# Kernel tuning notes

Measured on AMD Instinct MI355X. Metric: run time of the kernel, lower is better.

## Reference

```python
import jax, jax.numpy as jnp
import numpy as np

BSZ = 5
PROJ = 1000
DET = 513
IMG = 362
NPIX = IMG * IMG          # 131044
NNZ = 20_000_000


def setup_inputs() -> dict:
    key = jax.random.key(0)
    k1, k2, k3, k4 = jax.random.split(key, 4)
    filtered_sino = jax.random.normal(k1, (BSZ, PROJ, DET, 1), dtype=jnp.float32)
    sp_vals = jax.random.uniform(k2, (NNZ,), dtype=jnp.float32)
    sp_rows = jax.random.randint(k3, (NNZ,), 0, NPIX, dtype=jnp.int32)
    sp_cols = jax.random.randint(k4, (NNZ,), 0, PROJ * DET, dtype=jnp.int32)
    return {"filtered_sino": filtered_sino, "sp_vals": sp_vals,
            "sp_rows": sp_rows, "sp_cols": sp_cols}


def reference(filtered_sino, sp_vals, sp_rows, sp_cols):
    # Flatten each sinogram to [PROJ*DET] (row-major: proj then det, as tf.reshape).
    sino_flat = filtered_sino.reshape(BSZ, PROJ * DET)

    def back_project(s):  # s: [PROJ*DET] -> [NPIX]
        # sparse COO @ dense vector: out[row] += val * s[col]
        return jax.ops.segment_sum(sp_vals * s[sp_cols], sp_rows, num_segments=NPIX)

    rec = jax.vmap(back_project)(sino_flat)          # [BSZ, NPIX]
    # sens_image = back-projection of an all-ones sinogram
    sens = jax.ops.segment_sum(sp_vals, sp_rows, num_segments=NPIX)  # [NPIX]
    out = (rec / sens).reshape(BSZ, IMG, IMG, 1)
    return out
```

## Files before the change

### kernel.cpp

```cpp
#include <hip/hip_runtime.h>
#include <hip/hip_fp16.h>

#define BSZ  5
#define PROJ 1000
#define DET  513
#define IMG  362
#define NPIX (IMG * IMG)
#define SINO (PROJ * DET)
#define NNZ  20000000

#define NSHARD     4
#define SHARD_COLS (SINO / NSHARD)
#define RB_SHIFT   10
#define RB_PX      1024
#define NRBIN      128
#define NBIN       (NRBIN * NSHARD)

#define SCAT_BLOCKS  256
#define CHUNK        78128
#define TILE         4096
#define SC2_THREADS  512

#define CAP        200
#define OVF_CAP    65536

#define ACC_THREADS  512

#define FXSCALE 16384.0f
#define FXINV   (1.0f / 16384.0f)
#define FXB     262144
#define NTAG    0x1000000u

typedef int      i32x4 __attribute__((ext_vector_type(4)));
typedef float    f32x4 __attribute__((ext_vector_type(4)));
typedef unsigned u32x4 __attribute__((ext_vector_type(4)));

__device__ __forceinline__ unsigned lds_off(const void* p) {
    return (unsigned)(size_t)p;
}
__device__ __forceinline__ void ds_add_u64_nr(unsigned off, unsigned long long v) {
    asm volatile("ds_add_u64 %0, %1" :: "v"(off), "v"(v) : "memory");
}
__device__ __forceinline__ void lgkm_drain() {
    asm volatile("s_waitcnt lgkmcnt(0)" ::: "memory");
}

__device__ __forceinline__ int bin_of(int row, int col) {
    return ((row >> RB_SHIFT) << 2) | (col / SHARD_COLS);
}


__global__ void k_sino_bf16(const float* __restrict__ sino, u32x4* __restrict__ sino_b) {
    const int c = blockIdx.x * blockDim.x + threadIdx.x;
    if (c < SINO) {
        unsigned b[5];
#pragma unroll
        for (int k = 0; k < 5; ++k) {
            const unsigned u = __float_as_uint(sino[(size_t)k * SINO + c]);
            b[k] = (u + 0x7FFFu + ((u >> 16) & 1u)) >> 16;
        }
        u32x4 o;
        o.x = b[0] | (b[1] << 16);
        o.y = b[2] | (b[3] << 16);
        o.z = b[4];
        o.w = 0u;
        sino_b[c] = o;
    }
}

__global__ __launch_bounds__(SC2_THREADS) void k_scatter(
        const float* __restrict__ vals, const int* __restrict__ rows,
        const int* __restrict__ cols,
        unsigned* __restrict__ recA, unsigned short* __restrict__ recB,
        unsigned* __restrict__ gcnt,
        unsigned long long* __restrict__ ovf, unsigned* __restrict__ ovf_n) {
    __shared__ unsigned cnt[NBIN];
    __shared__ unsigned toff[NBIN];
    __shared__ unsigned ebase[NBIN];
    __shared__ unsigned bs2[NBIN];
    __shared__ unsigned wsum[8];
    __shared__ unsigned long long sdata[TILE];
    const int t = threadIdx.x;
    const int lane = t & 63;
    const int lo = blockIdx.x * CHUNK;
    const int hi = (lo + CHUNK < NNZ) ? lo + CHUNK : NNZ;
    if (lo >= hi) return;

    if (t < NBIN) {
        bs2[t] = ((unsigned)blockIdx.x * NBIN + (unsigned)t) * CAP;
        cnt[t] = 0u;
    }

    i32x4 sr0, sr1, sq0, sq1; f32x4 sv0, sv1;
    {
        const int n0 = (lo + TILE < hi) ? TILE : (hi - lo);
        if (t * 8 < n0) {
            const int i4 = (lo + t * 8) >> 2;
            sr0 = __builtin_nontemporal_load(((const i32x4*)rows) + i4);
            sr1 = __builtin_nontemporal_load(((const i32x4*)rows) + i4 + 1);
            sq0 = __builtin_nontemporal_load(((const i32x4*)cols) + i4);
            sq1 = __builtin_nontemporal_load(((const i32x4*)cols) + i4 + 1);
            sv0 = __builtin_nontemporal_load(((const f32x4*)vals) + i4);
            sv1 = __builtin_nontemporal_load(((const f32x4*)vals) + i4 + 1);
        }
    }
    __syncthreads();

    for (int tb = lo; tb < hi; tb += TILE) {
        const int n = (tb + TILE < hi) ? TILE : (hi - tb);
        const bool act = (t * 8) < n;

        const i32x4 cr0 = sr0, cr1 = sr1, cq0 = sq0, cq1 = sq1;
        const f32x4 cv0 = sv0, cv1 = sv1;

        const int ntb = tb + TILE;
        if (ntb < hi) {
            const int nn = (ntb + TILE < hi) ? TILE : (hi - ntb);
            if (t * 8 < nn) {
                const int i4 = (ntb + t * 8) >> 2;
                sr0 = __builtin_nontemporal_load(((const i32x4*)rows) + i4);
                sr1 = __builtin_nontemporal_load(((const i32x4*)rows) + i4 + 1);
                sq0 = __builtin_nontemporal_load(((const i32x4*)cols) + i4);
                sq1 = __builtin_nontemporal_load(((const i32x4*)cols) + i4 + 1);
                sv0 = __builtin_nontemporal_load(((const f32x4*)vals) + i4);
                sv1 = __builtin_nontemporal_load(((const f32x4*)vals) + i4 + 1);
            }
        }

        unsigned long long r8[8];
        unsigned sl[8];
        if (act) {
#pragma unroll
            for (int k = 0; k < 8; ++k) {
                const int rr = (k < 4) ? cr0[k] : cr1[k - 4];
                const int qq = (k < 4) ? cq0[k] : cq1[k - 4];
                const float vf = (k < 4) ? cv0[k] : cv1[k - 4];
                const unsigned bn = (unsigned)bin_of(rr, qq);
                const unsigned vh = (unsigned)__half_as_ushort(__float2half(vf));
                r8[k] = ((unsigned long long)bn << 55)
                      | ((unsigned long long)(unsigned)(rr & (RB_PX - 1)) << 45)
                      | ((unsigned long long)(unsigned)qq << 26)
                      | (unsigned long long)vh;
                sl[k] = atomicAdd(&cnt[bn], 1u);
            }
        }
        __syncthreads();

        unsigned x = 0u, incl = 0u;
        if (t < NBIN) {
            x = cnt[t];
            incl = x;
#pragma unroll
            for (int o = 1; o < 64; o <<= 1) {
                const unsigned y = __shfl_up(incl, (unsigned)o, 64);
                if (lane >= o) incl += y;
            }
            if (lane == 63) wsum[t >> 6] = incl;
        }
        __syncthreads();
        if (t < NBIN) {
            unsigned wo = 0u;
            const int w = t >> 6;
            for (int k = 0; k < w; ++k) wo += wsum[k];
            const unsigned e = wo + incl - x;
            toff[t] = e;
            ebase[t] = bs2[t] - e;
            bs2[t] += x;
            cnt[t] = 0u;
        }
        __syncthreads();

        if (act) {
#pragma unroll
            for (int k = 0; k < 8; ++k) {
                const unsigned bn = (unsigned)(r8[k] >> 55);
                sdata[toff[bn] + sl[k]] = r8[k];
            }
        }
        __syncthreads();

        for (int j = t; j < n; j += SC2_THREADS) {
            const unsigned long long u = sdata[j];
            const unsigned sb = (unsigned)(u >> 55);
            const unsigned pos = ebase[sb] + (unsigned)j;
            const unsigned cb = ((unsigned)blockIdx.x * NBIN + sb) * CAP;
            const unsigned pk = (unsigned)((u >> 26) & 0x1FFFFFFFu);
            const unsigned short vh = (unsigned short)(u & 0xFFFFu);
            if (pos - cb < CAP) {
                recA[pos] = pk;
                recB[pos] = vh;
            } else {
                const unsigned g = atomicAdd(ovf_n, 1u);
                if (g < OVF_CAP) ovf[g] = u;
            }
        }
        __syncthreads();
    }

    if (t < NBIN) {
        const unsigned cb = ((unsigned)blockIdx.x * NBIN + (unsigned)t) * CAP;
        const unsigned total = bs2[t] - cb;
        gcnt[(size_t)blockIdx.x * NBIN + t] = (total < CAP) ? total : CAP;
    }
}

__global__ __launch_bounds__(ACC_THREADS) void k_accum(
        const unsigned* __restrict__ recA, const unsigned short* __restrict__ recB,
        const unsigned* __restrict__ gcnt, const u32x4* __restrict__ sino_b,
        float* __restrict__ acc) {
    __shared__ unsigned long long l8[RB_PX * 3];
    __shared__ unsigned fcnt[SCAT_BLOCKS];
    const int t = threadIdx.x;
    const int bin = blockIdx.x;
    for (int j = t; j < RB_PX * 3; j += ACC_THREADS) l8[j] = 0ull;
    if (t < SCAT_BLOCKS) fcnt[t] = gcnt[(size_t)t * NBIN + bin];
    __syncthreads();

    const int w = t >> 6, lane = t & 63;
    for (int f = w; f < SCAT_BLOCKS; f += 8) {
        const unsigned n = fcnt[f];
        const unsigned base = ((unsigned)f * NBIN + (unsigned)bin) * CAP;
        for (unsigned j = (unsigned)lane; j < n; j += 64) {
            const unsigned a = recA[base + j];
            const float v = __half2float(__ushort_as_half(recB[base + j]));
            const int col = (int)(a & 0x7FFFFu);
            const int lr  = (int)(a >> 19);
            const u32x4 sv = sino_b[col];
            const int q0 = __float2int_rn(v * __uint_as_float(sv.x << 16)         * FXSCALE);
            const int q1 = __float2int_rn(v * __uint_as_float(sv.x & 0xFFFF0000u) * FXSCALE);
            const int q2 = __float2int_rn(v * __uint_as_float(sv.y << 16)         * FXSCALE);
            const int q3 = __float2int_rn(v * __uint_as_float(sv.y & 0xFFFF0000u) * FXSCALE);
            const int q4 = __float2int_rn(v * __uint_as_float(sv.z << 16)         * FXSCALE);
            const int q5 = __float2int_rn(v * FXSCALE);
            const unsigned b = lds_off(&l8[(unsigned)lr * 3u]);
            ds_add_u64_nr(b,
                ((unsigned long long)(unsigned)q1 << 32) | (unsigned)(q0 + FXB));
            ds_add_u64_nr(b + 8,
                ((unsigned long long)(unsigned)q3 << 32) | (unsigned)(q2 + FXB));
            ds_add_u64_nr(b + 16,
                ((unsigned long long)((unsigned)q5 + NTAG) << 32) | (unsigned)(q4 + FXB));
        }
    }
    lgkm_drain();
    __syncthreads();
    float* dst = acc + (size_t)bin * (RB_PX * 6);
    for (int px = t; px < RB_PX; px += ACC_THREADS) {
        const unsigned long long a0 = l8[px * 3 + 0];
        const unsigned long long a1 = l8[px * 3 + 1];
        const unsigned long long a2 = l8[px * 3 + 2];
        const unsigned hi3 = (unsigned)(a2 >> 32);
        const unsigned n = hi3 >> 24;
        const long long nb = (long long)n * FXB;
        float* d = dst + px * 6;
        d[0] = (float)((long long)(unsigned)(a0 & 0xFFFFFFFFull) - nb) * FXINV;
        d[1] = (float)((int)(a0 >> 32)) * FXINV;
        d[2] = (float)((long long)(unsigned)(a1 & 0xFFFFFFFFull) - nb) * FXINV;
        d[3] = (float)((int)(a1 >> 32)) * FXINV;
        d[4] = (float)((long long)(unsigned)(a2 & 0xFFFFFFFFull) - nb) * FXINV;
        d[5] = (float)(hi3 & 0xFFFFFFu) * FXINV;
    }
}

__global__ void k_fixup(const unsigned long long* __restrict__ ovf,
                        const unsigned* __restrict__ ovf_n,
                        const u32x4* __restrict__ sino_b,
                        float* __restrict__ acc) {
    unsigned n = *ovf_n;
    if (n > OVF_CAP) n = OVF_CAP;
    for (unsigned i = threadIdx.x; i < n; i += blockDim.x) {
        const unsigned long long u = ovf[i];
        const unsigned sb = (unsigned)(u >> 55);
        const unsigned pk = (unsigned)((u >> 26) & 0x1FFFFFFFu);
        const float v = __half2float(__ushort_as_half((unsigned short)(u & 0xFFFFu)));
        const int col = (int)(pk & 0x7FFFFu);
        const int lr  = (int)(pk >> 19);
        const u32x4 sv = sino_b[col];
        float* d = acc + (size_t)sb * (RB_PX * 6) + (size_t)lr * 6;
        atomicAdd(d + 0, v * __uint_as_float(sv.x << 16));
        atomicAdd(d + 1, v * __uint_as_float(sv.x & 0xFFFF0000u));
        atomicAdd(d + 2, v * __uint_as_float(sv.y << 16));
        atomicAdd(d + 3, v * __uint_as_float(sv.y & 0xFFFF0000u));
        atomicAdd(d + 4, v * __uint_as_float(sv.z << 16));
        atomicAdd(d + 5, v);
    }
}

__global__ void k_reduce(const float* __restrict__ acc, float* __restrict__ out) {
    const int p = blockIdx.x * blockDim.x + threadIdx.x;
    if (p < NPIX) {
        const int rbin = p >> RB_SHIFT, lr = p & (RB_PX - 1);
        float n0 = 0.f, n1 = 0.f, n2 = 0.f, n3 = 0.f, n4 = 0.f, den = 0.f;
#pragma unroll
        for (int s = 0; s < NSHARD; ++s) {
            const float* b = acc + ((size_t)(rbin * NSHARD + s) * RB_PX + lr) * 6;
            n0 += b[0]; n1 += b[1]; n2 += b[2];
            n3 += b[3]; n4 += b[4]; den += b[5];
        }
        const float inv = 1.f / den;
        out[0 * (size_t)NPIX + p] = n0 * inv;
        out[1 * (size_t)NPIX + p] = n1 * inv;
        out[2 * (size_t)NPIX + p] = n2 * inv;
        out[3 * (size_t)NPIX + p] = n3 * inv;
        out[4 * (size_t)NPIX + p] = n4 * inv;
    }
}


__global__ void bp_scatter_fb_kernel(const float* __restrict__ sino,
                                     const float* __restrict__ vals,
                                     const int*   __restrict__ rows,
                                     const int*   __restrict__ cols,
                                     float* __restrict__ acc) {
    const long long stride = (long long)gridDim.x * blockDim.x;
    for (long long i = (long long)blockIdx.x * blockDim.x + threadIdx.x;
         i < NNZ; i += stride) {
        const float v = vals[i];
        const int   r = rows[i];
        const int   c = cols[i];
        atomicAdd(acc + (size_t)BSZ * NPIX + r, v);
#pragma unroll
        for (int b = 0; b < BSZ; ++b)
            atomicAdd(acc + (size_t)b * NPIX + r, v * sino[(size_t)b * SINO + c]);
    }
}

__global__ void bp_divide_fb_kernel(const float* __restrict__ acc,
                                    float* __restrict__ out) {
    const int i = blockIdx.x * blockDim.x + threadIdx.x;
    if (i < BSZ * NPIX) {
        const int p = i % NPIX;
        out[i] = acc[i] / acc[(size_t)BSZ * NPIX + p];
    }
}


extern "C" void kernel_launch(void* const* d_in, const int* in_sizes, int n_in,
                              void* d_out, int out_size, void* d_ws, size_t ws_size,
                              hipStream_t stream) {
    const float* sino = (const float*)d_in[0];
    const float* vals = (const float*)d_in[1];
    const int*   rows = (const int*)d_in[2];
    const int*   cols = (const int*)d_in[3];
    float* out = (float*)d_out;

    const size_t recA_b   = (size_t)SCAT_BLOCKS * NBIN * CAP * 4;
    const size_t recB_b   = (size_t)SCAT_BLOCKS * NBIN * CAP * 2;
    const size_t sino_b_b = (size_t)SINO * 16;
    const size_t acc_b    = (size_t)NBIN * RB_PX * 6 * 4;
    const size_t gcnt_b   = (size_t)SCAT_BLOCKS * NBIN * 4;
    const size_t ovf_b    = (size_t)OVF_CAP * 8;
    const size_t need = recA_b + recB_b + sino_b_b + acc_b + gcnt_b + ovf_b + 16;

    if (ws_size >= need) {
        char* w = (char*)d_ws;
        unsigned*       recA = (unsigned*)w;                w += recA_b;
        unsigned short* recB = (unsigned short*)w;          w += recB_b;
        u32x4*    sinob  = (u32x4*)w;                       w += sino_b_b;
        float*    acc    = (float*)w;                       w += acc_b;
        unsigned* gcnt   = (unsigned*)w;                    w += gcnt_b;
        unsigned long long* ovf = (unsigned long long*)w;   w += ovf_b;
        unsigned* ovf_n  = (unsigned*)w;

        (void)hipMemsetAsync(ovf_n, 0, 4, stream);
        k_sino_bf16<<<(SINO + 255) / 256, 256, 0, stream>>>(sino, sinob);
        k_scatter<<<SCAT_BLOCKS, SC2_THREADS, 0, stream>>>(
            vals, rows, cols, recA, recB, gcnt, ovf, ovf_n);
        k_accum<<<NBIN, ACC_THREADS, 0, stream>>>(recA, recB, gcnt, sinob, acc);
        k_fixup<<<1, 256, 0, stream>>>(ovf, ovf_n, sinob, acc);
        k_reduce<<<(NPIX + 255) / 256, 256, 0, stream>>>(acc, out);
    } else {
        float* acc = (float*)d_ws;
        (void)hipMemsetAsync(acc, 0, (size_t)(BSZ + 1) * NPIX * sizeof(float), stream);
        bp_scatter_fb_kernel<<<2048, 256, 0, stream>>>(sino, vals, rows, cols, acc);
        bp_divide_fb_kernel<<<(BSZ * NPIX + 255) / 256, 256, 0, stream>>>(acc, out);
    }
}
```

Baseline: 250.3 us.

## Fuse sinogram bf16 packing into scatter, bin-major record layout, fold overflow into accum

Moves the bf16 sinogram packing into the start of the scatter kernel (256 blocks x 512 threads x 4 columns covers all sinogram columns) and removes a separate launch. Record storage changes to bin-major order, so each accumulate block reads one contiguous region with a flat strided loop and masks unused slots, instead of looping per fragment with a warp. The single-block overflow fixup kernel is removed; each accumulate block scans the overflow list and adds its own bin's entries into LDS. This costs every block a full scan of the overflow list and reads of padded, empty slots.

```diff
diff --git a/kernel.cpp b/kernel.cpp
--- a/kernel.cpp
+++ b/kernel.cpp
@@ -22,6 +22,7 @@
 #define SC2_THREADS  512
 
 #define CAP        200
+#define CELLS_PER_BIN (SCAT_BLOCKS * CAP)
 #define OVF_CAP    65536
 
 #define ACC_THREADS  512
@@ -50,25 +51,8 @@
 }
 
 
-__global__ void k_sino_bf16(const float* __restrict__ sino, u32x4* __restrict__ sino_b) {
-    const int c = blockIdx.x * blockDim.x + threadIdx.x;
-    if (c < SINO) {
-        unsigned b[5];
-#pragma unroll
-        for (int k = 0; k < 5; ++k) {
-            const unsigned u = __float_as_uint(sino[(size_t)k * SINO + c]);
-            b[k] = (u + 0x7FFFu + ((u >> 16) & 1u)) >> 16;
-        }
-        u32x4 o;
-        o.x = b[0] | (b[1] << 16);
-        o.y = b[2] | (b[3] << 16);
-        o.z = b[4];
-        o.w = 0u;
-        sino_b[c] = o;
-    }
-}
-
 __global__ __launch_bounds__(SC2_THREADS) void k_scatter(
+        const float* __restrict__ sino, u32x4* __restrict__ sino_b,
         const float* __restrict__ vals, const int* __restrict__ rows,
         const int* __restrict__ cols,
         unsigned* __restrict__ recA, unsigned short* __restrict__ recB,
@@ -82,12 +66,35 @@
     __shared__ unsigned long long sdata[TILE];
     const int t = threadIdx.x;
     const int lane = t & 63;
+
+    {
+        const int cbase = blockIdx.x * (SC2_THREADS * 4) + t * 4;
+#pragma unroll
+        for (int k = 0; k < 4; ++k) {
+            const int c = cbase + k;
+            if (c < SINO) {
+                unsigned b[5];
+#pragma unroll
+                for (int j = 0; j < 5; ++j) {
+                    const unsigned u = __float_as_uint(sino[(size_t)j * SINO + c]);
+                    b[j] = (u + 0x7FFFu + ((u >> 16) & 1u)) >> 16;
+                }
+                u32x4 o;
+                o.x = b[0] | (b[1] << 16);
+                o.y = b[2] | (b[3] << 16);
+                o.z = b[4];
+                o.w = 0u;
+                sino_b[c] = o;
+            }
+        }
+    }
+
     const int lo = blockIdx.x * CHUNK;
     const int hi = (lo + CHUNK < NNZ) ? lo + CHUNK : NNZ;
     if (lo >= hi) return;
 
     if (t < NBIN) {
-        bs2[t] = ((unsigned)blockIdx.x * NBIN + (unsigned)t) * CAP;
+        bs2[t] = ((unsigned)t * SCAT_BLOCKS + (unsigned)blockIdx.x) * CAP;
         cnt[t] = 0u;
     }
 
@@ -183,7 +190,7 @@
             const unsigned long long u = sdata[j];
             const unsigned sb = (unsigned)(u >> 55);
             const unsigned pos = ebase[sb] + (unsigned)j;
-            const unsigned cb = ((unsigned)blockIdx.x * NBIN + sb) * CAP;
+            const unsigned cb = (sb * SCAT_BLOCKS + (unsigned)blockIdx.x) * CAP;
             const unsigned pk = (unsigned)((u >> 26) & 0x1FFFFFFFu);
             const unsigned short vh = (unsigned short)(u & 0xFFFFu);
             if (pos - cb < CAP) {
@@ -198,7 +205,7 @@
     }
 
     if (t < NBIN) {
-        const unsigned cb = ((unsigned)blockIdx.x * NBIN + (unsigned)t) * CAP;
+        const unsigned cb = ((unsigned)t * SCAT_BLOCKS + (unsigned)blockIdx.x) * CAP;
         const unsigned total = bs2[t] - cb;
         gcnt[(size_t)blockIdx.x * NBIN + t] = (total < CAP) ? total : CAP;
     }
@@ -207,6 +214,7 @@
 __global__ __launch_bounds__(ACC_THREADS) void k_accum(
         const unsigned* __restrict__ recA, const unsigned short* __restrict__ recB,
         const unsigned* __restrict__ gcnt, const u32x4* __restrict__ sino_b,
+        const unsigned long long* __restrict__ ovf, const unsigned* __restrict__ ovf_n,
         float* __restrict__ acc) {
     __shared__ unsigned long long l8[RB_PX * 3];
     __shared__ unsigned fcnt[SCAT_BLOCKS];
@@ -216,13 +224,14 @@
     if (t < SCAT_BLOCKS) fcnt[t] = gcnt[(size_t)t * NBIN + bin];
     __syncthreads();
 
-    const int w = t >> 6, lane = t & 63;
-    for (int f = w; f < SCAT_BLOCKS; f += 8) {
-        const unsigned n = fcnt[f];
-        const unsigned base = ((unsigned)f * NBIN + (unsigned)bin) * CAP;
-        for (unsigned j = (unsigned)lane; j < n; j += 64) {
-            const unsigned a = recA[base + j];
-            const float v = __half2float(__ushort_as_half(recB[base + j]));
+    const unsigned binbase = (unsigned)bin * CELLS_PER_BIN;
+    for (unsigned i = (unsigned)t; i < CELLS_PER_BIN; i += ACC_THREADS) {
+        const unsigned frag = i / CAP;
+        const unsigned slot = i - frag * CAP;
+        const unsigned a = recA[binbase + i];
+        const unsigned short hraw = recB[binbase + i];
+        if (slot < fcnt[frag]) {
+            const float v = __half2float(__ushort_as_half(hraw));
             const int col = (int)(a & 0x7FFFFu);
             const int lr  = (int)(a >> 19);
             const u32x4 sv = sino_b[col];
@@ -241,8 +250,36 @@
                 ((unsigned long long)((unsigned)q5 + NTAG) << 32) | (unsigned)(q4 + FXB));
         }
     }
+
+    {
+        unsigned n = *ovf_n;
+        if (n > OVF_CAP) n = OVF_CAP;
+        for (unsigned i = (unsigned)t; i < n; i += ACC_THREADS) {
+            const unsigned long long u = ovf[i];
+            if ((unsigned)(u >> 55) != (unsigned)bin) continue;
+            const float v = __half2float(__ushort_as_half((unsigned short)(u & 0xFFFFu)));
+            const unsigned pk = (unsigned)((u >> 26) & 0x1FFFFFFFu);
+            const int col = (int)(pk & 0x7FFFFu);
+            const int lr  = (int)(pk >> 19);
+            const u32x4 sv = sino_b[col];
+            const int q0 = __float2int_rn(v * __uint_as_float(sv.x << 16)         * FXSCALE);
+            const int q1 = __float2int_rn(v * __uint_as_float(sv.x & 0xFFFF0000u) * FXSCALE);
+            const int q2 = __float2int_rn(v * __uint_as_float(sv.y << 16)         * FXSCALE);
+            const int q3 = __float2int_rn(v * __uint_as_float(sv.y & 0xFFFF0000u) * FXSCALE);
+            const int q4 = __float2int_rn(v * __uint_as_float(sv.z << 16)         * FXSCALE);
+            const int q5 = __float2int_rn(v * FXSCALE);
+            const unsigned b = lds_off(&l8[(unsigned)lr * 3u]);
+            ds_add_u64_nr(b,
+                ((unsigned long long)(unsigned)q1 << 32) | (unsigned)(q0 + FXB));
+            ds_add_u64_nr(b + 8,
+                ((unsigned long long)(unsigned)q3 << 32) | (unsigned)(q2 + FXB));
+            ds_add_u64_nr(b + 16,
+                ((unsigned long long)((unsigned)q5 + NTAG) << 32) | (unsigned)(q4 + FXB));
+        }
+    }
     lgkm_drain();
     __syncthreads();
+
     float* dst = acc + (size_t)bin * (RB_PX * 6);
     for (int px = t; px < RB_PX; px += ACC_THREADS) {
         const unsigned long long a0 = l8[px * 3 + 0];
@@ -261,30 +298,6 @@
     }
 }
 
-__global__ void k_fixup(const unsigned long long* __restrict__ ovf,
-                        const unsigned* __restrict__ ovf_n,
-                        const u32x4* __restrict__ sino_b,
-                        float* __restrict__ acc) {
-    unsigned n = *ovf_n;
-    if (n > OVF_CAP) n = OVF_CAP;
-    for (unsigned i = threadIdx.x; i < n; i += blockDim.x) {
-        const unsigned long long u = ovf[i];
-        const unsigned sb = (unsigned)(u >> 55);
-        const unsigned pk = (unsigned)((u >> 26) & 0x1FFFFFFFu);
-        const float v = __half2float(__ushort_as_half((unsigned short)(u & 0xFFFFu)));
-        const int col = (int)(pk & 0x7FFFFu);
-        const int lr  = (int)(pk >> 19);
-        const u32x4 sv = sino_b[col];
-        float* d = acc + (size_t)sb * (RB_PX * 6) + (size_t)lr * 6;
-        atomicAdd(d + 0, v * __uint_as_float(sv.x << 16));
-        atomicAdd(d + 1, v * __uint_as_float(sv.x & 0xFFFF0000u));
-        atomicAdd(d + 2, v * __uint_as_float(sv.y << 16));
-        atomicAdd(d + 3, v * __uint_as_float(sv.y & 0xFFFF0000u));
-        atomicAdd(d + 4, v * __uint_as_float(sv.z << 16));
-        atomicAdd(d + 5, v);
-    }
-}
-
 __global__ void k_reduce(const float* __restrict__ acc, float* __restrict__ out) {
     const int p = blockIdx.x * blockDim.x + threadIdx.x;
     if (p < NPIX) {
@@ -343,8 +356,8 @@
     const int*   cols = (const int*)d_in[3];
     float* out = (float*)d_out;
 
-    const size_t recA_b   = (size_t)SCAT_BLOCKS * NBIN * CAP * 4;
-    const size_t recB_b   = (size_t)SCAT_BLOCKS * NBIN * CAP * 2;
+    const size_t recA_b   = (size_t)NBIN * CELLS_PER_BIN * 4;
+    const size_t recB_b   = (size_t)NBIN * CELLS_PER_BIN * 2;
     const size_t sino_b_b = (size_t)SINO * 16;
     const size_t acc_b    = (size_t)NBIN * RB_PX * 6 * 4;
     const size_t gcnt_b   = (size_t)SCAT_BLOCKS * NBIN * 4;
@@ -362,11 +375,10 @@
         unsigned* ovf_n  = (unsigned*)w;
 
         (void)hipMemsetAsync(ovf_n, 0, 4, stream);
-        k_sino_bf16<<<(SINO + 255) / 256, 256, 0, stream>>>(sino, sinob);
         k_scatter<<<SCAT_BLOCKS, SC2_THREADS, 0, stream>>>(
-            vals, rows, cols, recA, recB, gcnt, ovf, ovf_n);
-        k_accum<<<NBIN, ACC_THREADS, 0, stream>>>(recA, recB, gcnt, sinob, acc);
-        k_fixup<<<1, 256, 0, stream>>>(ovf, ovf_n, sinob, acc);
+            sino, sinob, vals, rows, cols, recA, recB, gcnt, ovf, ovf_n);
+        k_accum<<<NBIN, ACC_THREADS, 0, stream>>>(
+            recA, recB, gcnt, sinob, ovf, ovf_n, acc);
         k_reduce<<<(NPIX + 255) / 256, 256, 0, stream>>>(acc, out);
     } else {
         float* acc = (float*)d_ws;
```

Measured after the change: 249.9 us. About the same (-0.1%).
